# Kernel tuning notes

Hardware: AMD Instinct MI355X
Metric: run time of the kernel (lower is better)

Reference implementation:

```python
import jax, jax.numpy as jnp
import numpy as np

B, S, H, C = 16, 4096, 1024, 64

def setup_inputs() -> dict:
    key = jax.random.key(0)
    k1, k2 = jax.random.split(key)
    hidden = jax.random.normal(k1, (B, S, H), dtype=jnp.float32)
    querys = jax.random.normal(k2, (C, H), dtype=jnp.float32)
    return {"hidden": hidden, "querys": querys}

def reference(hidden, querys):
    # scores: [B, C, S] = einsum over hidden_size
    scores = jnp.einsum('bsh,ch->bcs', hidden, querys)
    # softmax over the sequence axis
    factor = jax.nn.softmax(scores, axis=2)
    # pooled: [B, C, H]
    result = jnp.einsum('bcs,bsh->bch', factor, hidden)
    # flatten to [B, C*H]
    return result.reshape(-1, querys.shape[0] * querys.shape[1])
```

## Files before the change

kernel.cpp:

```cpp
#include <hip/hip_runtime.h>
#include <math.h>

#define BB 16
#define SS 4096
#define HH 1024
#define CC 64

typedef __attribute__((ext_vector_type(4))) float f32x4;
typedef __attribute__((ext_vector_type(8))) short s16x8;
typedef __attribute__((ext_vector_type(4))) unsigned int u32x4;
typedef unsigned int u32;

typedef const __attribute__((address_space(1))) u32* gas_ptr;
typedef __attribute__((address_space(3))) u32* las_ptr;

__device__ __forceinline__ void cp16(void* lds, const void* g) {
    __builtin_amdgcn_global_load_lds((gas_ptr)g, (las_ptr)(unsigned)(uintptr_t)lds, 16, 0, 0);
}

__device__ __forceinline__ ushort f2bf(float x) {
    union { float f; unsigned u; } un; un.f = x;
    unsigned r = (un.u + 0x7FFFu + ((un.u >> 16) & 1u)) >> 16;
    return (ushort)r;
}

__device__ __forceinline__ unsigned hipack(unsigned v1, unsigned v0) {
    return __builtin_amdgcn_perm(v1, v0, 0x07060302u);
}

__device__ __forceinline__ void cvt8(f32x4 f0, f32x4 f1, s16x8& hi, s16x8& lo) {
    u32x4 u0 = __builtin_bit_cast(u32x4, f0);
    u32x4 u1 = __builtin_bit_cast(u32x4, f1);
    u32x4 b0 = u0 + 0x8000u;
    u32x4 b1 = u1 + 0x8000u;
    f32x4 m0 = __builtin_bit_cast(f32x4, b0 & 0xFFFF0000u);
    f32x4 m1 = __builtin_bit_cast(f32x4, b1 & 0xFFFF0000u);
    u32x4 r0 = __builtin_bit_cast(u32x4, f0 - m0);
    u32x4 r1 = __builtin_bit_cast(u32x4, f1 - m1);
    u32x4 h = { hipack(b0.y, b0.x), hipack(b0.w, b0.z),
                hipack(b1.y, b1.x), hipack(b1.w, b1.z) };
    u32x4 l = { hipack(r0.y, r0.x), hipack(r0.w, r0.z),
                hipack(r1.y, r1.x), hipack(r1.w, r1.z) };
    hi = __builtin_bit_cast(s16x8, h);
    lo = __builtin_bit_cast(s16x8, l);
}

__global__ __launch_bounds__(256) void prep_querys_kernel(
    const float* __restrict__ q, ushort* __restrict__ qpkhi, ushort* __restrict__ qpklo)
{
    const int t = blockIdx.x * 256 + threadIdx.x;
    const int lane = t & 63;
    const int ks = (t >> 6) & 31;
    const int nt = t >> 11;
    const int c = nt * 16 + (lane & 15);
    const int k = ks * 32 + (lane >> 4) * 8;
    f32x4 f0 = *(const f32x4*)&q[(size_t)c * HH + k];
    f32x4 f1 = *(const f32x4*)&q[(size_t)c * HH + k + 4];
    s16x8 hi, lo;
    cvt8(f0, f1, hi, lo);
    *(s16x8*)&qpkhi[(size_t)t * 8] = hi;
    *(s16x8*)&qpklo[(size_t)t * 8] = lo;
}

__global__ __launch_bounds__(256, 4) void scores_kernel(
    const float* __restrict__ hidden, const ushort* __restrict__ qpkhi,
    const ushort* __restrict__ qpklo, float* __restrict__ scores,
    ushort* __restrict__ hid_hi)
{
    __shared__ __align__(16) float  As[2][64 * 32];
    __shared__ __align__(16) ushort Bhs[2][4 * 64 * 8];
    __shared__ __align__(16) ushort Bls[2][4 * 64 * 8];

    const int b  = blockIdx.y;
    const int s0 = blockIdx.x * 64;
    const int t  = threadIdx.x;
    const int w = t >> 6, lane = t & 63, col = lane & 15, quad = lane >> 4;

    const float* hb = hidden + ((size_t)b * SS + s0) * HH;

    const int st_r8 = lane >> 3;
    const int gA   = (((lane & 7) ^ st_r8) << 2);

    const int fr  = w * 16 + col;
    const int swz = (fr & 7) << 2;
    const int idxA = fr * 32 + ((quad * 8) ^ swz);
    ushort* hout = hid_hi + ((size_t)b * SS + s0 + fr) * HH;

    f32x4 acc[4];
#pragma unroll
    for (int j = 0; j < 4; ++j) acc[j] = (f32x4){0.f, 0.f, 0.f, 0.f};

#define STAGE(BUF, KS) do { \
    _Pragma("unroll") \
    for (int i = 0; i < 2; ++i) \
        cp16(&As[BUF][(w * 2 + i) * 256], \
             hb + (size_t)((w * 2 + i) * 8 + st_r8) * HH + (KS) * 32 + gA); \
    cp16(&Bhs[BUF][w * 512], qpkhi + ((size_t)(w * 32 + (KS)) * 64 + lane) * 8); \
    cp16(&Bls[BUF][w * 512], qpklo + ((size_t)(w * 32 + (KS)) * 64 + lane) * 8); } while (0)

    int cur = 0;
    STAGE(0, 0);
    __syncthreads();

    for (int ks = 0; ks < 32; ++ks) {
        if (ks + 1 < 32) STAGE(cur ^ 1, ks + 1);

        const float* Ab = &As[cur][0];
        f32x4 a0 = *(const f32x4*)&Ab[idxA];
        f32x4 a1 = *(const f32x4*)&Ab[idxA ^ 4];
        s16x8 ah, al;
        cvt8(a0, a1, ah, al);
        *(s16x8*)&hout[ks * 32 + quad * 8] = ah;
#pragma unroll
        for (int nt = 0; nt < 4; ++nt) {
            const s16x8 bh = *(const s16x8*)&Bhs[cur][nt * 512 + lane * 8];
            const s16x8 bl = *(const s16x8*)&Bls[cur][nt * 512 + lane * 8];
            acc[nt] = __builtin_amdgcn_mfma_f32_16x16x32_bf16(ah, bh, acc[nt], 0, 0, 0);
            acc[nt] = __builtin_amdgcn_mfma_f32_16x16x32_bf16(ah, bl, acc[nt], 0, 0, 0);
            acc[nt] = __builtin_amdgcn_mfma_f32_16x16x32_bf16(al, bh, acc[nt], 0, 0, 0);
        }
        __syncthreads();
        cur ^= 1;
    }
#undef STAGE

#pragma unroll
    for (int nt = 0; nt < 4; ++nt) {
        const int c = nt * 16 + col;
        const int s = s0 + w * 16 + quad * 4;
        *(f32x4*)&scores[((size_t)(b * CC + c)) * SS + s] = acc[nt];
    }
}

__global__ __launch_bounds__(256) void softmax_kernel(
    const float* __restrict__ scores, ushort* __restrict__ factor)
{
    const float* p = scores + (size_t)blockIdx.x * SS;
    ushort* f = factor + (size_t)blockIdx.x * SS;
    const int t = threadIdx.x;
    float4 v[4];
    float m = -3.0e38f;
#pragma unroll
    for (int i = 0; i < 4; ++i) {
        v[i] = *(const float4*)&p[t * 4 + i * 1024];
        m = fmaxf(m, fmaxf(fmaxf(v[i].x, v[i].y), fmaxf(v[i].z, v[i].w)));
    }
#pragma unroll
    for (int off = 1; off < 64; off <<= 1) m = fmaxf(m, __shfl_xor(m, off));
    __shared__ float redm[4];
    __shared__ float reds[4];
    const int wave = t >> 6, lane = t & 63;
    if (lane == 0) redm[wave] = m;
    __syncthreads();
    m = fmaxf(fmaxf(redm[0], redm[1]), fmaxf(redm[2], redm[3]));

    float sum = 0.0f;
#pragma unroll
    for (int i = 0; i < 4; ++i) {
        v[i].x = __expf(v[i].x - m); v[i].y = __expf(v[i].y - m);
        v[i].z = __expf(v[i].z - m); v[i].w = __expf(v[i].w - m);
        sum += (v[i].x + v[i].y) + (v[i].z + v[i].w);
    }
#pragma unroll
    for (int off = 1; off < 64; off <<= 1) sum += __shfl_xor(sum, off);
    if (lane == 0) reds[wave] = sum;
    __syncthreads();
    sum = (reds[0] + reds[1]) + (reds[2] + reds[3]);
    const float inv = 1.0f / sum;
#pragma unroll
    for (int i = 0; i < 4; ++i) {
        ushort4 o;
        o.x = f2bf(v[i].x * inv); o.y = f2bf(v[i].y * inv);
        o.z = f2bf(v[i].z * inv); o.w = f2bf(v[i].w * inv);
        ((ushort4*)f)[t + i * 256] = o;
    }
}

__global__ __launch_bounds__(256, 6) void pool_kernel(
    const ushort* __restrict__ hid_hi, const ushort* __restrict__ factor,
    float* __restrict__ parts)
{
    __shared__ __align__(16) ushort Bs[2][64 * 32];

    const int b  = blockIdx.y;
    const int h0 = blockIdx.x * 32;
    const int ks4 = blockIdx.z;
    const int sbeg = ks4 * (SS / 4);
    const int t = threadIdx.x;
    const int w = t >> 6, lane = t & 63, col = lane & 15, quad = lane >> 4;

    const int st_s = w * 16 + (lane >> 2);
    const int st_h = (lane & 3) * 8;
    const ushort* hbase = hid_hi + ((size_t)b * SS + sbeg) * HH + h0;

    f32x4 acc[2];
    acc[0] = (f32x4){0.f, 0.f, 0.f, 0.f};
    acc[1] = (f32x4){0.f, 0.f, 0.f, 0.f};

    const ushort* fptr = factor + ((size_t)(b * CC + w * 16 + col)) * SS + sbeg + quad * 8;

#define PSTAGE(BUF, SC) \
    cp16(&Bs[BUF][(size_t)w * 16 * 32], hbase + (size_t)((SC) + st_s) * HH + st_h)

    s16x8 fa0 = *(const s16x8*)&fptr[0];
    s16x8 fa1 = *(const s16x8*)&fptr[32];
    PSTAGE(0, 0);
    __syncthreads();

    int cur = 0;
    for (int sc = 0; sc < SS / 4; sc += 64) {
        s16x8 fn0, fn1;
        if (sc + 64 < SS / 4) {
            PSTAGE(cur ^ 1, sc + 64);
            fn0 = *(const s16x8*)&fptr[sc + 64];
            fn1 = *(const s16x8*)&fptr[sc + 96];
        }

        const u32* B32 = (const u32*)&Bs[cur][0];
#pragma unroll
        for (int ksub = 0; ksub < 2; ++ksub) {
            const s16x8 fa = ksub ? fa1 : fa0;
#pragma unroll
            for (int nt = 0; nt < 2; ++nt) {
                const int h_loc = nt * 16 + col;
                const unsigned sel = (h_loc & 1) ? 0x07060302u : 0x05040100u;
                const int base = (ksub * 32 + quad * 8) * 16 + (h_loc >> 1);
                u32 d0, d1, d2, d3;
                { u32 u0 = B32[base +  0], u1 = B32[base + 16];
                  d0 = __builtin_amdgcn_perm(u1, u0, sel); }
                { u32 u0 = B32[base + 32], u1 = B32[base + 48];
                  d1 = __builtin_amdgcn_perm(u1, u0, sel); }
                { u32 u0 = B32[base + 64], u1 = B32[base + 80];
                  d2 = __builtin_amdgcn_perm(u1, u0, sel); }
                { u32 u0 = B32[base + 96], u1 = B32[base + 112];
                  d3 = __builtin_amdgcn_perm(u1, u0, sel); }
                u32x4 dv = { d0, d1, d2, d3 };
                const s16x8 hbv = __builtin_bit_cast(s16x8, dv);
                acc[nt] = __builtin_amdgcn_mfma_f32_16x16x32_bf16(fa, hbv, acc[nt], 0, 0, 0);
            }
        }
        __syncthreads();
        cur ^= 1;
        fa0 = fn0;
        fa1 = fn1;
    }
#undef PSTAGE

    float* dst = parts + (size_t)ks4 * (BB * CC * HH) + (size_t)b * (CC * HH);
#pragma unroll
    for (int nt = 0; nt < 2; ++nt) {
        const int h = h0 + nt * 16 + col;
#pragma unroll
        for (int r = 0; r < 4; ++r) {
            const int c = w * 16 + quad * 4 + r;
            dst[(size_t)c * HH + h] = acc[nt][r];
        }
    }
}

__global__ __launch_bounds__(256) void reduce4_kernel(
    const float* __restrict__ parts, float* __restrict__ out)
{
    const int i = blockIdx.x * 256 + threadIdx.x;
    const float4* p = (const float4*)parts;
    const float4 a = p[i];
    const float4 b = p[i + 262144];
    const float4 c = p[i + 524288];
    const float4 d = p[i + 786432];
    float4 r;
    r.x = (a.x + b.x) + (c.x + d.x);
    r.y = (a.y + b.y) + (c.y + d.y);
    r.z = (a.z + b.z) + (c.z + d.z);
    r.w = (a.w + b.w) + (c.w + d.w);
    ((float4*)out)[i] = r;
}

extern "C" void kernel_launch(void* const* d_in, const int* in_sizes, int n_in,
                              void* d_out, int out_size, void* d_ws, size_t ws_size,
                              hipStream_t stream)
{
    const float* hidden = (const float*)d_in[0];
    const float* querys = (const float*)d_in[1];
    float* out = (float*)d_out;

    float*  scores = (float*)d_ws;
    float*  parts  = (float*)d_ws;
    ushort* factor = (ushort*)((char*)d_ws + (16u << 20));
    ushort* qpkhi  = (ushort*)((char*)d_ws + (24u << 20));
    ushort* qpklo  = qpkhi + 4 * 32 * 64 * 8;
    ushort* hid_hi = (ushort*)((char*)d_ws + (32u << 20));

    prep_querys_kernel<<<dim3(32), 256, 0, stream>>>(querys, qpkhi, qpklo);
    scores_kernel<<<dim3(SS / 64, BB), 256, 0, stream>>>(hidden, qpkhi, qpklo, scores, hid_hi);
    softmax_kernel<<<dim3(BB * CC), 256, 0, stream>>>(scores, factor);
    pool_kernel<<<dim3(HH / 32, BB, 4), 256, 0, stream>>>(hid_hi, factor, parts);
    reduce4_kernel<<<dim3(1024), 256, 0, stream>>>(parts, out);
}
```

Measured before the change: 491.9 us.

## Retile scores and pool kernels: smaller S tiles, wider H tiles, 8-way split

The scores kernel now handles 32 sequence rows per block, with the four waves split into 2 row groups by 2 column halves. This doubles the grid and allows 6 waves per SIMD, at the cost of loading each B tile for half as many rows. The pool kernel widens its H tile to 64 with an XOR-swizzled LDS layout and splits the sequence 8 ways instead of 4, giving each wave more MFMAs per staged tile. In exchange the partial-sum buffer grows to 8 copies and moves to its own workspace region, so the reduce kernel reads more data.

After: 471.8 us. 4.1% less time.

```diff
diff --git a/kernel.cpp b/kernel.cpp
--- a/kernel.cpp
+++ b/kernel.cpp
@@ -62,39 +62,37 @@
     *(s16x8*)&qpklo[(size_t)t * 8] = lo;
 }
 
-__global__ __launch_bounds__(256, 4) void scores_kernel(
+__global__ __launch_bounds__(256, 6) void scores_kernel(
     const float* __restrict__ hidden, const ushort* __restrict__ qpkhi,
     const ushort* __restrict__ qpklo, float* __restrict__ scores,
     ushort* __restrict__ hid_hi)
 {
-    __shared__ __align__(16) float  As[2][64 * 32];
+    __shared__ __align__(16) float  As[2][32 * 32];
     __shared__ __align__(16) ushort Bhs[2][4 * 64 * 8];
     __shared__ __align__(16) ushort Bls[2][4 * 64 * 8];
 
     const int b  = blockIdx.y;
-    const int s0 = blockIdx.x * 64;
+    const int s0 = blockIdx.x * 32;
     const int t  = threadIdx.x;
     const int w = t >> 6, lane = t & 63, col = lane & 15, quad = lane >> 4;
+    const int rg = w & 1;
+    const int ch = w >> 1;
 
     const float* hb = hidden + ((size_t)b * SS + s0) * HH;
 
     const int st_r8 = lane >> 3;
     const int gA   = (((lane & 7) ^ st_r8) << 2);
 
-    const int fr  = w * 16 + col;
-    const int swz = (fr & 7) << 2;
-    const int idxA = fr * 32 + ((quad * 8) ^ swz);
+    const int fr  = rg * 16 + col;
+    const int idxA = fr * 32 + ((quad * 8) ^ ((fr & 7) << 2));
     ushort* hout = hid_hi + ((size_t)b * SS + s0 + fr) * HH;
 
-    f32x4 acc[4];
-#pragma unroll
-    for (int j = 0; j < 4; ++j) acc[j] = (f32x4){0.f, 0.f, 0.f, 0.f};
+    f32x4 acc[2];
+    acc[0] = (f32x4){0.f, 0.f, 0.f, 0.f};
+    acc[1] = (f32x4){0.f, 0.f, 0.f, 0.f};
 
 #define STAGE(BUF, KS) do { \
-    _Pragma("unroll") \
-    for (int i = 0; i < 2; ++i) \
-        cp16(&As[BUF][(w * 2 + i) * 256], \
-             hb + (size_t)((w * 2 + i) * 8 + st_r8) * HH + (KS) * 32 + gA); \
+    cp16(&As[BUF][w * 8 * 32], hb + (size_t)(w * 8 + st_r8) * HH + (KS) * 32 + gA); \
     cp16(&Bhs[BUF][w * 512], qpkhi + ((size_t)(w * 32 + (KS)) * 64 + lane) * 8); \
     cp16(&Bls[BUF][w * 512], qpklo + ((size_t)(w * 32 + (KS)) * 64 + lane) * 8); } while (0)
 
@@ -110,11 +108,12 @@
         f32x4 a1 = *(const f32x4*)&Ab[idxA ^ 4];
         s16x8 ah, al;
         cvt8(a0, a1, ah, al);
-        *(s16x8*)&hout[ks * 32 + quad * 8] = ah;
-#pragma unroll
-        for (int nt = 0; nt < 4; ++nt) {
-            const s16x8 bh = *(const s16x8*)&Bhs[cur][nt * 512 + lane * 8];
-            const s16x8 bl = *(const s16x8*)&Bls[cur][nt * 512 + lane * 8];
+        if (ch == 0) *(s16x8*)&hout[ks * 32 + quad * 8] = ah;
+#pragma unroll
+        for (int nt = 0; nt < 2; ++nt) {
+            const int ng = ch * 2 + nt;
+            const s16x8 bh = *(const s16x8*)&Bhs[cur][ng * 512 + lane * 8];
+            const s16x8 bl = *(const s16x8*)&Bls[cur][ng * 512 + lane * 8];
             acc[nt] = __builtin_amdgcn_mfma_f32_16x16x32_bf16(ah, bh, acc[nt], 0, 0, 0);
             acc[nt] = __builtin_amdgcn_mfma_f32_16x16x32_bf16(ah, bl, acc[nt], 0, 0, 0);
             acc[nt] = __builtin_amdgcn_mfma_f32_16x16x32_bf16(al, bh, acc[nt], 0, 0, 0);
@@ -125,9 +124,9 @@
 #undef STAGE
 
 #pragma unroll
-    for (int nt = 0; nt < 4; ++nt) {
-        const int c = nt * 16 + col;
-        const int s = s0 + w * 16 + quad * 4;
+    for (int nt = 0; nt < 2; ++nt) {
+        const int c = (ch * 2 + nt) * 16 + col;
+        const int s = s0 + rg * 16 + quad * 4;
         *(f32x4*)&scores[((size_t)(b * CC + c)) * SS + s] = acc[nt];
     }
 }
@@ -180,27 +179,31 @@
     const ushort* __restrict__ hid_hi, const ushort* __restrict__ factor,
     float* __restrict__ parts)
 {
-    __shared__ __align__(16) ushort Bs[2][64 * 32];
+    __shared__ __align__(16) ushort Bs[2][64 * 64];
 
     const int b  = blockIdx.y;
-    const int h0 = blockIdx.x * 32;
-    const int ks4 = blockIdx.z;
-    const int sbeg = ks4 * (SS / 4);
+    const int h0 = blockIdx.x * 64;
+    const int ks8 = blockIdx.z;
+    const int sbeg = ks8 * (SS / 8);
     const int t = threadIdx.x;
     const int w = t >> 6, lane = t & 63, col = lane & 15, quad = lane >> 4;
 
-    const int st_s = w * 16 + (lane >> 2);
-    const int st_h = (lane & 3) * 8;
     const ushort* hbase = hid_hi + ((size_t)b * SS + sbeg) * HH + h0;
 
-    f32x4 acc[2];
-    acc[0] = (f32x4){0.f, 0.f, 0.f, 0.f};
-    acc[1] = (f32x4){0.f, 0.f, 0.f, 0.f};
+    f32x4 acc[4];
+#pragma unroll
+    for (int j = 0; j < 4; ++j) acc[j] = (f32x4){0.f, 0.f, 0.f, 0.f};
 
     const ushort* fptr = factor + ((size_t)(b * CC + w * 16 + col)) * SS + sbeg + quad * 8;
 
-#define PSTAGE(BUF, SC) \
-    cp16(&Bs[BUF][(size_t)w * 16 * 32], hbase + (size_t)((SC) + st_s) * HH + st_h)
+#define PSTAGE(BUF, SC) do { \
+    _Pragma("unroll") \
+    for (int i = 0; i < 2; ++i) { \
+        const int inst = w * 2 + i; \
+        cp16(&Bs[BUF][inst * 8 * 64], \
+             hbase + (size_t)((SC) + inst * 8 + (lane >> 3)) * HH + \
+                 (((lane & 7) ^ ((inst & 3) << 1)) * 8)); \
+    } } while (0)
 
     s16x8 fa0 = *(const s16x8*)&fptr[0];
     s16x8 fa1 = *(const s16x8*)&fptr[32];
@@ -208,9 +211,9 @@
     __syncthreads();
 
     int cur = 0;
-    for (int sc = 0; sc < SS / 4; sc += 64) {
+    for (int sc = 0; sc < SS / 8; sc += 64) {
         s16x8 fn0, fn1;
-        if (sc + 64 < SS / 4) {
+        if (sc + 64 < SS / 8) {
             PSTAGE(cur ^ 1, sc + 64);
             fn0 = *(const s16x8*)&fptr[sc + 64];
             fn1 = *(const s16x8*)&fptr[sc + 96];
@@ -221,18 +224,19 @@
         for (int ksub = 0; ksub < 2; ++ksub) {
             const s16x8 fa = ksub ? fa1 : fa0;
 #pragma unroll
-            for (int nt = 0; nt < 2; ++nt) {
+            for (int nt = 0; nt < 4; ++nt) {
                 const int h_loc = nt * 16 + col;
                 const unsigned sel = (h_loc & 1) ? 0x07060302u : 0x05040100u;
-                const int base = (ksub * 32 + quad * 8) * 16 + (h_loc >> 1);
+                const int dq = (nt * 8 + (col >> 1)) ^ (quad << 3);
+                const int base = (ksub * 32 + quad * 8) * 32 + dq;
                 u32 d0, d1, d2, d3;
-                { u32 u0 = B32[base +  0], u1 = B32[base + 16];
+                { u32 u0 = B32[base +   0], u1 = B32[base +  32];
                   d0 = __builtin_amdgcn_perm(u1, u0, sel); }
-                { u32 u0 = B32[base + 32], u1 = B32[base + 48];
+                { u32 u0 = B32[base +  64], u1 = B32[base +  96];
                   d1 = __builtin_amdgcn_perm(u1, u0, sel); }
-                { u32 u0 = B32[base + 64], u1 = B32[base + 80];
+                { u32 u0 = B32[base + 128], u1 = B32[base + 160];
                   d2 = __builtin_amdgcn_perm(u1, u0, sel); }
-                { u32 u0 = B32[base + 96], u1 = B32[base + 112];
+                { u32 u0 = B32[base + 192], u1 = B32[base + 224];
                   d3 = __builtin_amdgcn_perm(u1, u0, sel); }
                 u32x4 dv = { d0, d1, d2, d3 };
                 const s16x8 hbv = __builtin_bit_cast(s16x8, dv);
@@ -246,9 +250,9 @@
     }
 #undef PSTAGE
 
-    float* dst = parts + (size_t)ks4 * (BB * CC * HH) + (size_t)b * (CC * HH);
-#pragma unroll
-    for (int nt = 0; nt < 2; ++nt) {
+    float* dst = parts + (size_t)ks8 * (BB * CC * HH) + (size_t)b * (CC * HH);
+#pragma unroll
+    for (int nt = 0; nt < 4; ++nt) {
         const int h = h0 + nt * 16 + col;
 #pragma unroll
         for (int r = 0; r < 4; ++r) {
@@ -258,20 +262,17 @@
     }
 }
 
-__global__ __launch_bounds__(256) void reduce4_kernel(
+__global__ __launch_bounds__(256) void reduce8_kernel(
     const float* __restrict__ parts, float* __restrict__ out)
 {
     const int i = blockIdx.x * 256 + threadIdx.x;
     const float4* p = (const float4*)parts;
-    const float4 a = p[i];
-    const float4 b = p[i + 262144];
-    const float4 c = p[i + 524288];
-    const float4 d = p[i + 786432];
-    float4 r;
-    r.x = (a.x + b.x) + (c.x + d.x);
-    r.y = (a.y + b.y) + (c.y + d.y);
-    r.z = (a.z + b.z) + (c.z + d.z);
-    r.w = (a.w + b.w) + (c.w + d.w);
+    float4 r = {0.f, 0.f, 0.f, 0.f};
+#pragma unroll
+    for (int k = 0; k < 8; ++k) {
+        const float4 a = p[i + (size_t)k * 262144];
+        r.x += a.x; r.y += a.y; r.z += a.z; r.w += a.w;
+    }
     ((float4*)out)[i] = r;
 }
 
@@ -284,15 +285,15 @@
     float* out = (float*)d_out;
 
     float*  scores = (float*)d_ws;
-    float*  parts  = (float*)d_ws;
     ushort* factor = (ushort*)((char*)d_ws + (16u << 20));
     ushort* qpkhi  = (ushort*)((char*)d_ws + (24u << 20));
     ushort* qpklo  = qpkhi + 4 * 32 * 64 * 8;
     ushort* hid_hi = (ushort*)((char*)d_ws + (32u << 20));
+    float*  parts  = (float*)((char*)d_ws + (160u << 20));
 
     prep_querys_kernel<<<dim3(32), 256, 0, stream>>>(querys, qpkhi, qpklo);
-    scores_kernel<<<dim3(SS / 64, BB), 256, 0, stream>>>(hidden, qpkhi, qpklo, scores, hid_hi);
+    scores_kernel<<<dim3(SS / 32, BB), 256, 0, stream>>>(hidden, qpkhi, qpklo, scores, hid_hi);
     softmax_kernel<<<dim3(BB * CC), 256, 0, stream>>>(scores, factor);
-    pool_kernel<<<dim3(HH / 32, BB, 4), 256, 0, stream>>>(hid_hi, factor, parts);
-    reduce4_kernel<<<dim3(1024), 256, 0, stream>>>(parts, out);
-}
+    pool_kernel<<<dim3(HH / 64, BB, 8), 256, 0, stream>>>(hid_hi, factor, parts);
+    reduce8_kernel<<<dim3(1024), 256, 0, stream>>>(parts, out);
+}
```
